# Optimization experiments

Measured on AMD Instinct MI355X. Metric: run time of the kernel, lower is better.

The kernel has to match this reference:

```python
import jax, jax.numpy as jnp
import numpy as np

D = 768; H = 12; DH = D // H; L = 12; FF = 3072; P = 20
IMG = (640, 360); NP_ = (IMG[0] // P) * (IMG[1] // P)  # 576 patches
NC = 10
EPS = 1e-5


def setup_inputs() -> dict:
    key = jax.random.key(0)
    ks = jax.random.split(key, 20)
    s = 0.02
    inp = {
        "x": jax.random.normal(ks[0], (16, 3, IMG[0], IMG[1]), jnp.float32),
        "patch_w": jax.random.normal(ks[1], (D, 3, P, P), jnp.float32) * s,
        "patch_b": jnp.zeros((D,), jnp.float32),
        "pos_emb": jax.random.normal(ks[2], (1, NP_, D), jnp.float32),
        "ln_g": jnp.ones((D,), jnp.float32),
        "ln_b": jnp.zeros((D,), jnp.float32),
        "Wq": jax.random.normal(ks[3], (L, D, D), jnp.float32) * s,
        "bq": jnp.zeros((L, D), jnp.float32),
        "Wk": jax.random.normal(ks[4], (L, D, D), jnp.float32) * s,
        "bk": jnp.zeros((L, D), jnp.float32),
        "Wv": jax.random.normal(ks[5], (L, D, D), jnp.float32) * s,
        "bv": jnp.zeros((L, D), jnp.float32),
        "Wo": jax.random.normal(ks[6], (L, D, D), jnp.float32) * s,
        "bo": jnp.zeros((L, D), jnp.float32),
        "W1": jax.random.normal(ks[7], (L, FF, D), jnp.float32) * s,
        "b1": jnp.zeros((L, FF), jnp.float32),
        "W2": jax.random.normal(ks[8], (L, D, FF), jnp.float32) * s,
        "b2": jnp.zeros((L, D), jnp.float32),
        "fc_w": jax.random.normal(ks[9], (NC, D), jnp.float32) * s,
        "fc_b": jnp.zeros((NC,), jnp.float32),
    }
    return inp


def _layer_norm(x, g, b):
    mu = jnp.mean(x, axis=-1, keepdims=True)
    var = jnp.mean(jnp.square(x - mu), axis=-1, keepdims=True)
    return (x - mu) * jax.lax.rsqrt(var + EPS) * g + b


def _forward(x, patch_w, patch_b, pos_emb, ln_g, ln_b,
             Wq, bq, Wk, bk, Wv, bv, Wo, bo, W1, b1, W2, b2, fc_w, fc_b):
    B = x.shape[0]
    Hp, Wp = IMG[0] // P, IMG[1] // P
    # patch embed: stride=kernel conv == per-patch linear
    patches = x.reshape(B, 3, Hp, P, Wp, P).transpose(0, 2, 4, 1, 3, 5)
    patches = patches.reshape(B, Hp * Wp, 3 * P * P)           # [B, N, 3*p*p]
    h = patches @ patch_w.reshape(D, -1).T + patch_b            # [B, N, D]
    h = h + pos_emb
    h = _layer_norm(h, ln_g, ln_b)

    def layer(h, p):
        wq, bq_, wk, bk_, wv, bv_, wo, bo_, w1, b1_, w2, b2_ = p
        N = h.shape[1]
        def heads(t):  # [B,N,D] -> [B,H,N,DH]
            return t.reshape(B, N, H, DH).transpose(0, 2, 1, 3)
        q = heads(h @ wq.T + bq_)
        k = heads(h @ wk.T + bk_)
        v = heads(h @ wv.T + bv_)
        scores = jnp.einsum('bhqd,bhkd->bhqk', q, k) / jnp.sqrt(jnp.float32(DH))
        attn = jax.nn.softmax(scores, axis=-1)
        o = jnp.einsum('bhqk,bhkd->bhqd', attn, v)
        o = o.transpose(0, 2, 1, 3).reshape(B, N, D) @ wo.T + bo_
        h = h + o
        ff = jax.nn.relu(h @ w1.T + b1_) @ w2.T + b2_
        return h + ff, None

    h, _ = jax.lax.scan(layer, h, (Wq, bq, Wk, bk, Wv, bv, Wo, bo, W1, b1, W2, b2))
    pooled = h.mean(axis=1)                                     # [B, D]
    return pooled @ fc_w.T + fc_b                               # [B, NC]


def reference(x, patch_w, patch_b, pos_emb, ln_g, ln_b,
              Wq, bq, Wk, bk, Wv, bv, Wo, bo, W1, b1, W2, b2, fc_w, fc_b):
    return _forward(x, patch_w, patch_b, pos_emb, ln_g, ln_b,
                    Wq, bq, Wk, bk, Wv, bv, Wo, bo, W1, b1, W2, b2, fc_w, fc_b)
```

## Files before the change

### kernel.cpp

```cpp
#include <hip/hip_runtime.h>
#include <stdint.h>
#include <stddef.h>

typedef __attribute__((ext_vector_type(8))) short short8;
typedef __attribute__((ext_vector_type(4))) float f32x4;

#define D_    768
#define HH    12
#define DHEAD 64
#define NP    576
#define BB    16
#define MROWS 9216
#define KPAT  1216
#define SCL   0.18033688011112042f

static __device__ __forceinline__ unsigned short f2bf(float f){
  union { float f; unsigned int u; } v; v.f = f;
  unsigned int u = v.u;
  return (unsigned short)((u + 0x7FFFu + ((u >> 16) & 1u)) >> 16);
}

static __device__ __forceinline__ void gld16(const void* g, void* l){
  __builtin_amdgcn_global_load_lds((const __attribute__((address_space(1))) void*)g,
                                   (__attribute__((address_space(3))) void*)l,
                                   16, 0, 0);
}

__global__ __launch_bounds__(256) void gemm_bt(
    const unsigned short* __restrict__ A,
    const unsigned short* __restrict__ W,
    const float* __restrict__ bias,
    const float* __restrict__ pos,
    const float* res,
    float* outf,
    unsigned short* outb,
    int M, int N, int K, int relu)
{
  __shared__ unsigned short sA[3][128*32];
  __shared__ unsigned short sB[3][128*32];
  const int NB = N >> 7;
  const int nwg = (int)gridDim.x;
  int wid = (int)blockIdx.x;
  wid = (wid & 7) * (nwg >> 3) + (wid >> 3);
  const int mb = wid / NB;
  const int nb = wid % NB;
  const int t = threadIdx.x;
  const int w = t >> 6, l = t & 63;
  const int m0 = mb << 7, n0 = nb << 7;

  const int srow = (w << 4) + (l >> 2);
  const int scb  = (l & 3) ^ ((l >> 3) & 3);
  const unsigned short* Ag = A + (size_t)(m0 + srow) * K + (scb << 3);
  const unsigned short* Wg = W + (size_t)(n0 + srow) * K + (scb << 3);
  const size_t g64 = (size_t)64 * K;

  const f32x4 zero = {0.f, 0.f, 0.f, 0.f};
  f32x4 acc[4][4];
  #pragma unroll
  for (int i = 0; i < 4; ++i)
    #pragma unroll
    for (int j = 0; j < 4; ++j) acc[i][j] = zero;

  const int KT = K >> 5;

  auto stage = [&](int kt){
    const int bf = kt % 3;
    const unsigned short* a0 = Ag + (size_t)kt * 32;
    const unsigned short* w0 = Wg + (size_t)kt * 32;
    gld16(a0,       &sA[bf][((w<<4) +  0)*32]);
    gld16(a0 + g64, &sA[bf][((w<<4) + 64)*32]);
    gld16(w0,       &sB[bf][((w<<4) +  0)*32]);
    gld16(w0 + g64, &sB[bf][((w<<4) + 64)*32]);
  };

  stage(0);
  stage(1);

  const int wr = w >> 1, wc = w & 1;
  const int fr = l & 15, fq = l >> 4;
  const int fsw = (fq ^ ((fr >> 1) & 3)) << 3;

  for (int kt = 0; kt < KT; ++kt){
    if (kt == KT - 1) asm volatile("s_waitcnt vmcnt(0) lgkmcnt(0)" ::: "memory");
    else              asm volatile("s_waitcnt vmcnt(4) lgkmcnt(0)" ::: "memory");
    __builtin_amdgcn_s_barrier();
    asm volatile("" ::: "memory");
    if (kt + 2 < KT) stage(kt + 2);
    const int buf = kt % 3;
    short8 af[4], bv[4];
    #pragma unroll
    for (int mf = 0; mf < 4; ++mf)
      af[mf] = *(const short8*)&sA[buf][((wr<<6) + (mf<<4) + fr)*32 + fsw];
    #pragma unroll
    for (int nf = 0; nf < 4; ++nf)
      bv[nf] = *(const short8*)&sB[buf][((wc<<6) + (nf<<4) + fr)*32 + fsw];
    #pragma unroll
    for (int mf = 0; mf < 4; ++mf)
      #pragma unroll
      for (int nf = 0; nf < 4; ++nf)
        acc[mf][nf] = __builtin_amdgcn_mfma_f32_16x16x32_bf16(af[mf], bv[nf], acc[mf][nf], 0, 0, 0);
    asm volatile("" ::: "memory");
  }

  #pragma unroll
  for (int mf = 0; mf < 4; ++mf){
    #pragma unroll
    for (int nf = 0; nf < 4; ++nf){
      #pragma unroll
      for (int r = 0; r < 4; ++r){
        const int row = m0 + (wr<<6) + (mf<<4) + (fq<<2) + r;
        const int col = n0 + (wc<<6) + (nf<<4) + fr;
        float v = acc[mf][nf][r] + bias[col];
        if (pos)  v += pos[(size_t)(row % NP) * D_ + col];
        if (res)  v += res[(size_t)row * N + col];
        if (relu) v = fmaxf(v, 0.f);
        const size_t idx = (size_t)row * N + col;
        if (outf) outf[idx] = v;
        if (outb) outb[idx] = f2bf(v);
      }
    }
  }
}

__global__ __launch_bounds__(384) void k_attn(const unsigned short* __restrict__ qkv,
                                              unsigned short* __restrict__ o)
{
  __shared__ unsigned short Kl[2][32*64];
  __shared__ unsigned short Vt[2][64*64];
  const int nwg = (int)gridDim.x;
  int wid = (int)blockIdx.x;
  wid = (wid & 7) * (nwg >> 3) + (wid >> 3);
  const int bh = wid / 3, qs = wid % 3;
  const int b = bh / HH, h = bh % HH;
  const unsigned short* base = qkv + (size_t)b * NP * 2304 + h * DHEAD;
  const int t = threadIdx.x;
  const int w = t >> 6, l = t & 63;
  const int fr = l & 15, fq = l >> 4;
  const int sg = l & 7;
  const int sr = ((w & 3) << 3) + (l >> 3);
  const bool stw = (t < 256);

  short8 qfa[2], qfb[2];
  #pragma unroll
  for (int qt = 0; qt < 2; ++qt){
    const size_t qrow = (size_t)(qs*192 + (qt*6 + w)*16 + fr);
    qfa[qt] = *(const short8*)(base + qrow*2304 + (fq<<3));
    qfb[qt] = *(const short8*)(base + qrow*2304 + 32 + (fq<<3));
  }

  const f32x4 zero = {0.f, 0.f, 0.f, 0.f};
  float mx_[2] = {-1e30f, -1e30f};
  float ls_[2] = {0.f, 0.f};
  f32x4 oa[2][4];
  #pragma unroll
  for (int qt = 0; qt < 2; ++qt)
    #pragma unroll
    for (int nf = 0; nf < 4; ++nf) oa[qt][nf] = zero;

  if (stw){
    gld16(base + 768 + (size_t)sr*2304 + ((sg ^ (sr&7))<<3), &Kl[0][(w&3)*512]);
    short8 vv = *(const short8*)(base + 1536 + (size_t)sr*2304 + (sg<<3));
    asm volatile("s_waitcnt vmcnt(0)" ::: "memory");
    #pragma unroll
    for (int j = 0; j < 8; ++j){
      const int d = sg*8 + j;
      const int off = (d<<7) + ((((sr>>3) ^ j ^ sg) & 7) << 4) + ((sr&7)<<1);
      *(unsigned short*)((char*)&Vt[0][0] + off) = ((const unsigned short*)&vv)[j];
    }
  }
  __syncthreads();

  for (int kt = 0; kt < 18; ++kt){
    const int buf = kt & 1;
    short8 vv;
    const bool st = stw && (kt < 17);
    if (st){
      const int key = (kt+1)*32 + sr;
      gld16(base + 768 + (size_t)key*2304 + ((sg ^ (sr&7))<<3), &Kl[buf^1][(w&3)*512]);
      vv = *(const short8*)(base + 1536 + (size_t)key*2304 + (sg<<3));
    }

    const char* kb = (const char*)&Kl[buf][0];
    const int r0 = fr, r1 = 16 + fr;
    const short8 k00 = *(const short8*)(kb + (r0<<7) + (((fq    ) ^ (r0&7))<<4));
    const short8 k01 = *(const short8*)(kb + (r0<<7) + (((4+fq ) ^ (r0&7))<<4));
    const short8 k10 = *(const short8*)(kb + (r1<<7) + (((fq    ) ^ (r1&7))<<4));
    const short8 k11 = *(const short8*)(kb + (r1<<7) + (((4+fq ) ^ (r1&7))<<4));
    const char* vb = (const char*)&Vt[buf][0];

    #pragma unroll
    for (int qt = 0; qt < 2; ++qt){
      f32x4 s0 = zero, s1 = zero;
      s0 = __builtin_amdgcn_mfma_f32_16x16x32_bf16(k00, qfa[qt], s0, 0, 0, 0);
      s0 = __builtin_amdgcn_mfma_f32_16x16x32_bf16(k01, qfb[qt], s0, 0, 0, 0);
      s1 = __builtin_amdgcn_mfma_f32_16x16x32_bf16(k10, qfa[qt], s1, 0, 0, 0);
      s1 = __builtin_amdgcn_mfma_f32_16x16x32_bf16(k11, qfb[qt], s1, 0, 0, 0);
      float mx = fmaxf(fmaxf(fmaxf(s0[0], s0[1]), fmaxf(s0[2], s0[3])),
                       fmaxf(fmaxf(s1[0], s1[1]), fmaxf(s1[2], s1[3])));
      mx = fmaxf(mx, __shfl_xor(mx, 16));
      mx = fmaxf(mx, __shfl_xor(mx, 32));
      const float mn = fmaxf(mx_[qt], mx * SCL);
      const float fc = exp2f(mx_[qt] - mn);
      const float p0 = exp2f(s0[0]*SCL - mn), p1 = exp2f(s0[1]*SCL - mn);
      const float p2 = exp2f(s0[2]*SCL - mn), p3 = exp2f(s0[3]*SCL - mn);
      const float p4 = exp2f(s1[0]*SCL - mn), p5 = exp2f(s1[1]*SCL - mn);
      const float p6 = exp2f(s1[2]*SCL - mn), p7 = exp2f(s1[3]*SCL - mn);
      float ps = ((p0+p1)+(p2+p3)) + ((p4+p5)+(p6+p7));
      ps += __shfl_xor(ps, 16);
      ps += __shfl_xor(ps, 32);
      ls_[qt] = ls_[qt] * fc + ps;
      mx_[qt] = mn;
      if (!__all(fc == 1.0f)){
        const float fA = __shfl(fc, (fq<<2) + 0);
        const float fB = __shfl(fc, (fq<<2) + 1);
        const float fC = __shfl(fc, (fq<<2) + 2);
        const float fD = __shfl(fc, (fq<<2) + 3);
        #pragma unroll
        for (int nf = 0; nf < 4; ++nf){
          oa[qt][nf][0] *= fA; oa[qt][nf][1] *= fB;
          oa[qt][nf][2] *= fC; oa[qt][nf][3] *= fD;
        }
      }
      unsigned d0, d1, d2, d3;
      asm("v_cvt_pk_bf16_f32 %0, %1, %2" : "=v"(d0) : "v"(p0), "v"(p1));
      asm("v_cvt_pk_bf16_f32 %0, %1, %2" : "=v"(d1) : "v"(p2), "v"(p3));
      asm("v_cvt_pk_bf16_f32 %0, %1, %2" : "=v"(d2) : "v"(p4), "v"(p5));
      asm("v_cvt_pk_bf16_f32 %0, %1, %2" : "=v"(d3) : "v"(p6), "v"(p7));
      const int srcA = fr + ((fq & 1) << 5);
      const unsigned a0 = (unsigned)__shfl((int)d0, srcA);
      const unsigned a1 = (unsigned)__shfl((int)d1, srcA);
      const unsigned a2 = (unsigned)__shfl((int)d2, srcA);
      const unsigned a3 = (unsigned)__shfl((int)d3, srcA);
      const unsigned b0 = (unsigned)__shfl((int)d0, srcA + 16);
      const unsigned b1 = (unsigned)__shfl((int)d1, srcA + 16);
      const unsigned b2 = (unsigned)__shfl((int)d2, srcA + 16);
      const unsigned b3 = (unsigned)__shfl((int)d3, srcA + 16);
      const bool hi = fq >= 2;
      union { unsigned u[4]; short8 v; } pk;
      pk.u[0] = hi ? a2 : a0;
      pk.u[1] = hi ? a3 : a1;
      pk.u[2] = hi ? b2 : b0;
      pk.u[3] = hi ? b3 : b1;
      const short8 pa = pk.v;
      #pragma unroll
      for (int nf = 0; nf < 4; ++nf){
        const int d = (nf<<4) + fr;
        const short8 vf = *(const short8*)(vb + (d<<7) + (((fq ^ (d&7) ^ (d>>3)) & 7)<<4));
        oa[qt][nf] = __builtin_amdgcn_mfma_f32_16x16x32_bf16(pa, vf, oa[qt][nf], 0, 0, 0);
      }
    }

    if (st){
      asm volatile("s_waitcnt vmcnt(0)" ::: "memory");
      #pragma unroll
      for (int j = 0; j < 8; ++j){
        const int d = sg*8 + j;
        const int off = (d<<7) + ((((sr>>3) ^ j ^ sg) & 7) << 4) + ((sr&7)<<1);
        *(unsigned short*)((char*)&Vt[buf^1][0] + off) = ((const unsigned short*)&vv)[j];
      }
    }
    __syncthreads();
  }

  #pragma unroll
  for (int qt = 0; qt < 2; ++qt){
    const float rl = 1.f / ls_[qt];
    const float rA = __shfl(rl, (fq<<2)+0), rB = __shfl(rl, (fq<<2)+1);
    const float rC = __shfl(rl, (fq<<2)+2), rD = __shfl(rl, (fq<<2)+3);
    const size_t r0 = (size_t)(b*NP + qs*192 + (qt*6 + w)*16 + (fq<<2));
    #pragma unroll
    for (int nf = 0; nf < 4; ++nf){
      const int col = h*DHEAD + (nf<<4) + fr;
      o[(r0 + 0)*D_ + col] = f2bf(oa[qt][nf][0] * rA);
      o[(r0 + 1)*D_ + col] = f2bf(oa[qt][nf][1] * rB);
      o[(r0 + 2)*D_ + col] = f2bf(oa[qt][nf][2] * rC);
      o[(r0 + 3)*D_ + col] = f2bf(oa[qt][nf][3] * rD);
    }
  }
}

__global__ void k_f2b(const float* __restrict__ s, unsigned short* __restrict__ d, long n){
  long i = (long)blockIdx.x * blockDim.x + threadIdx.x;
  const long st = (long)gridDim.x * blockDim.x;
  for (; i < n; i += st) d[i] = f2bf(s[i]);
}

__global__ void k_pack_qkvw(const float* __restrict__ Wq, const float* __restrict__ Wk,
                            const float* __restrict__ Wv, unsigned short* __restrict__ dst){
  const long n = (long)12 * 2304 * 768;
  long i = (long)blockIdx.x * blockDim.x + threadIdx.x;
  const long st = (long)gridDim.x * blockDim.x;
  for (; i < n; i += st){
    const int lay = (int)(i / (2304 * 768));
    const int rem = (int)(i % (2304 * 768));
    const int r = rem / 768, k = rem % 768;
    const float* s = (r < 768) ? Wq : ((r < 1536) ? Wk : Wv);
    const int rr = (r < 768) ? r : ((r < 1536) ? r - 768 : r - 1536);
    dst[i] = f2bf(s[(size_t)lay * 589824 + (size_t)rr * 768 + k]);
  }
}

__global__ void k_pack_qkvb(const float* __restrict__ bq, const float* __restrict__ bk,
                            const float* __restrict__ bv, float* __restrict__ dst){
  const int i = blockIdx.x * 256 + threadIdx.x;
  if (i >= 12 * 2304) return;
  const int lay = i / 2304, r = i % 2304;
  const float* s = (r < 768) ? bq : ((r < 1536) ? bk : bv);
  const int rr = (r < 768) ? r : ((r < 1536) ? r - 768 : r - 1536);
  dst[i] = s[lay * 768 + rr];
}

__global__ void k_patchw(const float* __restrict__ s, unsigned short* __restrict__ d){
  const long n = (long)768 * KPAT;
  long i = (long)blockIdx.x * blockDim.x + threadIdx.x;
  const long st = (long)gridDim.x * blockDim.x;
  for (; i < n; i += st){
    const int r = (int)(i / KPAT), k = (int)(i % KPAT);
    d[i] = (k < 1200) ? f2bf(s[(size_t)r * 1200 + k]) : (unsigned short)0;
  }
}

__global__ void k_patches(const float* __restrict__ x, unsigned short* __restrict__ d){
  const long n = (long)MROWS * KPAT;
  long i = (long)blockIdx.x * blockDim.x + threadIdx.x;
  const long st = (long)gridDim.x * blockDim.x;
  for (; i < n; i += st){
    const int mrow = (int)(i / KPAT), k = (int)(i % KPAT);
    unsigned short v = 0;
    if (k < 1200){
      const int c = k / 400, rem = k % 400, py = rem / 20, px = rem % 20;
      const int b = mrow / NP, pn = mrow % NP, hp = pn / 18, wp = pn % 18;
      v = f2bf(x[(((size_t)b * 3 + c) * 640 + hp * 20 + py) * 360 + wp * 20 + px]);
    }
    d[i] = v;
  }
}

__global__ __launch_bounds__(256) void k_ln(float* h, unsigned short* hb,
                                            const float* __restrict__ g,
                                            const float* __restrict__ bt){
  const int r = blockIdx.x, t = threadIdx.x;
  const size_t base = (size_t)r * D_;
  const float x0 = h[base + t], x1 = h[base + t + 256], x2 = h[base + t + 512];
  float s = x0 + x1 + x2;
  #pragma unroll
  for (int o = 1; o < 64; o <<= 1) s += __shfl_xor(s, o);
  __shared__ float red[8];
  const int w = t >> 6, l = t & 63;
  if (l == 0) red[w] = s;
  __syncthreads();
  const float mu = (red[0] + red[1] + red[2] + red[3]) * (1.f / 768.f);
  const float d0 = x0 - mu, d1 = x1 - mu, d2 = x2 - mu;
  float v = d0*d0 + d1*d1 + d2*d2;
  #pragma unroll
  for (int o = 1; o < 64; o <<= 1) v += __shfl_xor(v, o);
  if (l == 0) red[4 + w] = v;
  __syncthreads();
  const float var = (red[4] + red[5] + red[6] + red[7]) * (1.f / 768.f);
  const float rs = rsqrtf(var + 1e-5f);
  const float y0 = d0 * rs * g[t]       + bt[t];
  const float y1 = d1 * rs * g[t + 256] + bt[t + 256];
  const float y2 = d2 * rs * g[t + 512] + bt[t + 512];
  h[base + t] = y0; h[base + t + 256] = y1; h[base + t + 512] = y2;
  hb[base + t] = f2bf(y0); hb[base + t + 256] = f2bf(y1); hb[base + t + 512] = f2bf(y2);
}

__global__ void k_pool(const float* __restrict__ h, float* __restrict__ p){
  const int i = blockIdx.x * 256 + threadIdx.x;
  const int b = i / D_, c = i % D_;
  const float* base = h + (size_t)b * NP * D_ + c;
  float s = 0.f;
  for (int n = 0; n < NP; ++n) s += base[(size_t)n * D_];
  p[i] = s * (1.f / 576.f);
}

__global__ __launch_bounds__(64) void k_fc(const float* __restrict__ p, const float* __restrict__ w,
                                           const float* __restrict__ bias, float* __restrict__ out){
  const int oi = blockIdx.x;
  const int b = oi / 10, j = oi % 10;
  const int l = threadIdx.x;
  float s = 0.f;
  for (int c = l; c < D_; c += 64) s += p[b * D_ + c] * w[j * D_ + c];
  #pragma unroll
  for (int o = 1; o < 64; o <<= 1) s += __shfl_xor(s, o);
  if (l == 0) out[oi] = s + bias[j];
}

extern "C" void kernel_launch(void* const* d_in, const int* in_sizes, int n_in,
                              void* d_out, int out_size, void* d_ws, size_t ws_size,
                              hipStream_t stream)
{
  const float* x       = (const float*)d_in[0];
  const float* patch_w = (const float*)d_in[1];
  const float* patch_b = (const float*)d_in[2];
  const float* pos_emb = (const float*)d_in[3];
  const float* ln_g    = (const float*)d_in[4];
  const float* ln_b    = (const float*)d_in[5];
  const float* Wq      = (const float*)d_in[6];
  const float* bq      = (const float*)d_in[7];
  const float* Wk      = (const float*)d_in[8];
  const float* bk      = (const float*)d_in[9];
  const float* Wv      = (const float*)d_in[10];
  const float* bv      = (const float*)d_in[11];
  const float* Wo      = (const float*)d_in[12];
  const float* bo      = (const float*)d_in[13];
  const float* W1      = (const float*)d_in[14];
  const float* b1      = (const float*)d_in[15];
  const float* W2      = (const float*)d_in[16];
  const float* b2      = (const float*)d_in[17];
  const float* fc_w    = (const float*)d_in[18];
  const float* fc_b    = (const float*)d_in[19];
  float* out = (float*)d_out;
  (void)in_sizes; (void)n_in; (void)out_size; (void)ws_size;

  char* ws = (char*)d_ws;
  size_t off = 0;
  auto alloc = [&](size_t bytes) -> char* {
    char* p = ws + off;
    off += (bytes + 255) & ~(size_t)255;
    return p;
  };
  unsigned short* wqkv    = (unsigned short*)alloc((size_t)12*2304*768*2);
  unsigned short* wo      = (unsigned short*)alloc((size_t)12*768*768*2);
  unsigned short* w1      = (unsigned short*)alloc((size_t)12*3072*768*2);
  unsigned short* w2      = (unsigned short*)alloc((size_t)12*768*3072*2);
  unsigned short* wp      = (unsigned short*)alloc((size_t)768*KPAT*2);
  float*          bqkv    = (float*)alloc((size_t)12*2304*4);
  unsigned short* patches = (unsigned short*)alloc((size_t)MROWS*KPAT*2);
  float*          hf      = (float*)alloc((size_t)MROWS*D_*4);
  unsigned short* hb      = (unsigned short*)alloc((size_t)MROWS*D_*2);
  unsigned short* qkvb    = (unsigned short*)alloc((size_t)MROWS*2304*2);
  unsigned short* ob      = (unsigned short*)alloc((size_t)MROWS*D_*2);
  unsigned short* ffb     = (unsigned short*)alloc((size_t)MROWS*3072*2);
  float*          pooled  = (float*)alloc((size_t)16*D_*4);

  k_pack_qkvw<<<2048, 256, 0, stream>>>(Wq, Wk, Wv, wqkv);
  k_pack_qkvb<<<(12*2304 + 255)/256, 256, 0, stream>>>(bq, bk, bv, bqkv);
  k_f2b<<<2048, 256, 0, stream>>>(Wo, wo, (long)12*768*768);
  k_f2b<<<2048, 256, 0, stream>>>(W1, w1, (long)12*3072*768);
  k_f2b<<<2048, 256, 0, stream>>>(W2, w2, (long)12*768*3072);
  k_patchw<<<2048, 256, 0, stream>>>(patch_w, wp);
  k_patches<<<2048, 256, 0, stream>>>(x, patches);

  gemm_bt<<<72*6, 256, 0, stream>>>(patches, wp, patch_b, pos_emb,
                                    nullptr, hf, nullptr, MROWS, 768, KPAT, 0);
  k_ln<<<MROWS, 256, 0, stream>>>(hf, hb, ln_g, ln_b);

  for (int l = 0; l < 12; ++l){
    gemm_bt<<<72*18, 256, 0, stream>>>(hb, wqkv + (size_t)l*2304*768, bqkv + l*2304,
                                       nullptr, nullptr, nullptr, qkvb, MROWS, 2304, 768, 0);
    k_attn<<<576, 384, 0, stream>>>(qkvb, ob);
    gemm_bt<<<72*6, 256, 0, stream>>>(ob, wo + (size_t)l*768*768, bo + l*768,
                                      nullptr, hf, hf, hb, MROWS, 768, 768, 0);
    gemm_bt<<<72*24, 256, 0, stream>>>(hb, w1 + (size_t)l*3072*768, b1 + (size_t)l*3072,
                                       nullptr, nullptr, nullptr, ffb, MROWS, 3072, 768, 1);
    gemm_bt<<<72*6, 256, 0, stream>>>(ffb, w2 + (size_t)l*768*3072, b2 + l*768,
                                      nullptr, hf, hf, hb, MROWS, 768, 3072, 0);
  }
  k_pool<<<48, 256, 0, stream>>>(hf, pooled);
  k_fc<<<160, 64, 0, stream>>>(pooled, fc_w, fc_b, out);
}
```

Before: 4.258 ms.

## Enlarge GEMM tile to 256x128 with K-step 64 and 8 waves

Reworks the bf16 GEMM to use 512-thread workgroups, each computing a 256x128 output tile with a 64-wide K step. The shared-memory layout changes to 64-column rows with an XOR swizzle. Global-to-LDS loads are reorganised to six per stage, and MFMA bursts are wrapped in s_setprio. The goal is more operand reuse per byte loaded and fewer barrier iterations. In exchange, about 147KB of LDS is needed, so only one block fits per CU, and grids get smaller.

```diff
diff --git a/kernel.cpp b/kernel.cpp
--- a/kernel.cpp
+++ b/kernel.cpp
@@ -26,7 +26,7 @@
                                    16, 0, 0);
 }
 
-__global__ __launch_bounds__(256) void gemm_bt(
+__global__ __launch_bounds__(512) void gemm_bt(
     const unsigned short* __restrict__ A,
     const unsigned short* __restrict__ W,
     const float* __restrict__ bias,
@@ -36,8 +36,8 @@
     unsigned short* outb,
     int M, int N, int K, int relu)
 {
-  __shared__ unsigned short sA[3][128*32];
-  __shared__ unsigned short sB[3][128*32];
+  __shared__ unsigned short sA[3][256*64];
+  __shared__ unsigned short sB[3][128*64];
   const int NB = N >> 7;
   const int nwg = (int)gridDim.x;
   int wid = (int)blockIdx.x;
@@ -46,13 +46,18 @@
   const int nb = wid % NB;
   const int t = threadIdx.x;
   const int w = t >> 6, l = t & 63;
-  const int m0 = mb << 7, n0 = nb << 7;
-
-  const int srow = (w << 4) + (l >> 2);
-  const int scb  = (l & 3) ^ ((l >> 3) & 3);
-  const unsigned short* Ag = A + (size_t)(m0 + srow) * K + (scb << 3);
-  const unsigned short* Wg = W + (size_t)(n0 + srow) * K + (scb << 3);
-  const size_t g64 = (size_t)64 * K;
+  const int m0 = mb << 8, n0 = nb << 7;
+
+  const int lr = l >> 3;
+  const int sch = (l & 7) ^ lr;
+  const unsigned short* aP[4];
+  const unsigned short* bP[2];
+  #pragma unroll
+  for (int i = 0; i < 4; ++i)
+    aP[i] = A + (size_t)(m0 + (((i<<3)+w)<<3) + lr) * K + (sch<<3);
+  #pragma unroll
+  for (int i = 0; i < 2; ++i)
+    bP[i] = W + (size_t)(n0 + (((i<<3)+w)<<3) + lr) * K + (sch<<3);
 
   const f32x4 zero = {0.f, 0.f, 0.f, 0.f};
   f32x4 acc[4][4];
@@ -61,16 +66,17 @@
     #pragma unroll
     for (int j = 0; j < 4; ++j) acc[i][j] = zero;
 
-  const int KT = K >> 5;
+  const int KT = K >> 6;
 
   auto stage = [&](int kt){
     const int bf = kt % 3;
-    const unsigned short* a0 = Ag + (size_t)kt * 32;
-    const unsigned short* w0 = Wg + (size_t)kt * 32;
-    gld16(a0,       &sA[bf][((w<<4) +  0)*32]);
-    gld16(a0 + g64, &sA[bf][((w<<4) + 64)*32]);
-    gld16(w0,       &sB[bf][((w<<4) +  0)*32]);
-    gld16(w0 + g64, &sB[bf][((w<<4) + 64)*32]);
+    const size_t ko = (size_t)kt << 6;
+    #pragma unroll
+    for (int i = 0; i < 4; ++i)
+      gld16(aP[i] + ko, &sA[bf][(((i<<3)+w)<<9)]);
+    #pragma unroll
+    for (int i = 0; i < 2; ++i)
+      gld16(bP[i] + ko, &sB[bf][(((i<<3)+w)<<9)]);
   };
 
   stage(0);
@@ -78,27 +84,36 @@
 
   const int wr = w >> 1, wc = w & 1;
   const int fr = l & 15, fq = l >> 4;
-  const int fsw = (fq ^ ((fr >> 1) & 3)) << 3;
 
   for (int kt = 0; kt < KT; ++kt){
-    if (kt == KT - 1) asm volatile("s_waitcnt vmcnt(0) lgkmcnt(0)" ::: "memory");
-    else              asm volatile("s_waitcnt vmcnt(4) lgkmcnt(0)" ::: "memory");
+    if (kt == KT - 1) asm volatile("s_waitcnt vmcnt(0)" ::: "memory");
+    else              asm volatile("s_waitcnt vmcnt(6)" ::: "memory");
     __builtin_amdgcn_s_barrier();
     asm volatile("" ::: "memory");
     if (kt + 2 < KT) stage(kt + 2);
     const int buf = kt % 3;
-    short8 af[4], bv[4];
-    #pragma unroll
-    for (int mf = 0; mf < 4; ++mf)
-      af[mf] = *(const short8*)&sA[buf][((wr<<6) + (mf<<4) + fr)*32 + fsw];
-    #pragma unroll
-    for (int nf = 0; nf < 4; ++nf)
-      bv[nf] = *(const short8*)&sB[buf][((wc<<6) + (nf<<4) + fr)*32 + fsw];
-    #pragma unroll
-    for (int mf = 0; mf < 4; ++mf)
-      #pragma unroll
-      for (int nf = 0; nf < 4; ++nf)
-        acc[mf][nf] = __builtin_amdgcn_mfma_f32_16x16x32_bf16(af[mf], bv[nf], acc[mf][nf], 0, 0, 0);
+    #pragma unroll
+    for (int kc = 0; kc < 2; ++kc){
+      const int ch = (kc << 2) + fq;
+      short8 af[4], bv[4];
+      #pragma unroll
+      for (int mf = 0; mf < 4; ++mf){
+        const int r = (wr<<6) + (mf<<4) + fr;
+        af[mf] = *(const short8*)&sA[buf][(r<<6) + ((ch ^ (r&7))<<3)];
+      }
+      #pragma unroll
+      for (int nf = 0; nf < 4; ++nf){
+        const int c = (wc<<6) + (nf<<4) + fr;
+        bv[nf] = *(const short8*)&sB[buf][(c<<6) + ((ch ^ (c&7))<<3)];
+      }
+      __builtin_amdgcn_s_setprio(1);
+      #pragma unroll
+      for (int mf = 0; mf < 4; ++mf)
+        #pragma unroll
+        for (int nf = 0; nf < 4; ++nf)
+          acc[mf][nf] = __builtin_amdgcn_mfma_f32_16x16x32_bf16(af[mf], bv[nf], acc[mf][nf], 0, 0, 0);
+      __builtin_amdgcn_s_setprio(0);
+    }
     asm volatile("" ::: "memory");
   }
 
@@ -442,19 +457,19 @@
   k_patchw<<<2048, 256, 0, stream>>>(patch_w, wp);
   k_patches<<<2048, 256, 0, stream>>>(x, patches);
 
-  gemm_bt<<<72*6, 256, 0, stream>>>(patches, wp, patch_b, pos_emb,
+  gemm_bt<<<36*6, 512, 0, stream>>>(patches, wp, patch_b, pos_emb,
                                     nullptr, hf, nullptr, MROWS, 768, KPAT, 0);
   k_ln<<<MROWS, 256, 0, stream>>>(hf, hb, ln_g, ln_b);
 
   for (int l = 0; l < 12; ++l){
-    gemm_bt<<<72*18, 256, 0, stream>>>(hb, wqkv + (size_t)l*2304*768, bqkv + l*2304,
+    gemm_bt<<<36*18, 512, 0, stream>>>(hb, wqkv + (size_t)l*2304*768, bqkv + l*2304,
                                        nullptr, nullptr, nullptr, qkvb, MROWS, 2304, 768, 0);
     k_attn<<<576, 384, 0, stream>>>(qkvb, ob);
-    gemm_bt<<<72*6, 256, 0, stream>>>(ob, wo + (size_t)l*768*768, bo + l*768,
+    gemm_bt<<<36*6, 512, 0, stream>>>(ob, wo + (size_t)l*768*768, bo + l*768,
                                       nullptr, hf, hf, hb, MROWS, 768, 768, 0);
-    gemm_bt<<<72*24, 256, 0, stream>>>(hb, w1 + (size_t)l*3072*768, b1 + (size_t)l*3072,
+    gemm_bt<<<36*24, 512, 0, stream>>>(hb, w1 + (size_t)l*3072*768, b1 + (size_t)l*3072,
                                        nullptr, nullptr, nullptr, ffb, MROWS, 3072, 768, 1);
-    gemm_bt<<<72*6, 256, 0, stream>>>(ffb, w2 + (size_t)l*768*3072, b2 + l*768,
+    gemm_bt<<<36*6, 512, 0, stream>>>(ffb, w2 + (size_t)l*768*3072, b2 + l*768,
                                       nullptr, hf, hf, hb, MROWS, 768, 3072, 0);
   }
   k_pool<<<48, 256, 0, stream>>>(hf, pooled);
```

New measurement: 4.582 ms. +7.6%, slower.

## Restructure GEMM to keep weight slab in LDS and stream A from global

Applied to the files above, without the earlier changes.

Rewrites the bf16 GEMM so each 512-thread block loads a 64-column by up-to-768-K slab of the weight matrix into a 128KB LDS buffer once, with an XOR swizzle. A fragments are then read directly from global memory into registers, software-pipelined four k-steps deep. Tiles become 256x64 instead of 128x128, and KPAT is padded to 1280 so the patch GEMM splits into 768-wide chunks. The aim is to remove the per-k-step LDS staging and barriers for A, at the cost of uncoalesced global A reads, very high LDS use that limits occupancy, and a changed padded patch layout.

```diff
diff --git a/kernel.cpp b/kernel.cpp
--- a/kernel.cpp
+++ b/kernel.cpp
@@ -11,7 +11,7 @@
 #define NP    576
 #define BB    16
 #define MROWS 9216
-#define KPAT  1216
+#define KPAT  1280
 #define SCL   0.18033688011112042f
 
 static __device__ __forceinline__ unsigned short f2bf(float f){
@@ -26,7 +26,7 @@
                                    16, 0, 0);
 }
 
-__global__ __launch_bounds__(256) void gemm_bt(
+__global__ __launch_bounds__(512) void gemm_bt(
     const unsigned short* __restrict__ A,
     const unsigned short* __restrict__ W,
     const float* __restrict__ bias,
@@ -36,9 +36,8 @@
     unsigned short* outb,
     int M, int N, int K, int relu)
 {
-  __shared__ unsigned short sA[3][128*32];
-  __shared__ unsigned short sB[3][128*32];
-  const int NB = N >> 7;
+  __shared__ unsigned short sW[64*1024];
+  const int NB = N >> 6;
   const int nwg = (int)gridDim.x;
   int wid = (int)blockIdx.x;
   wid = (wid & 7) * (nwg >> 3) + (wid >> 3);
@@ -46,70 +45,80 @@
   const int nb = wid % NB;
   const int t = threadIdx.x;
   const int w = t >> 6, l = t & 63;
-  const int m0 = mb << 7, n0 = nb << 7;
-
-  const int srow = (w << 4) + (l >> 2);
-  const int scb  = (l & 3) ^ ((l >> 3) & 3);
-  const unsigned short* Ag = A + (size_t)(m0 + srow) * K + (scb << 3);
-  const unsigned short* Wg = W + (size_t)(n0 + srow) * K + (scb << 3);
-  const size_t g64 = (size_t)64 * K;
-
-  const f32x4 zero = {0.f, 0.f, 0.f, 0.f};
-  f32x4 acc[4][4];
-  #pragma unroll
-  for (int i = 0; i < 4; ++i)
-    #pragma unroll
-    for (int j = 0; j < 4; ++j) acc[i][j] = zero;
-
-  const int KT = K >> 5;
-
-  auto stage = [&](int kt){
-    const int bf = kt % 3;
-    const unsigned short* a0 = Ag + (size_t)kt * 32;
-    const unsigned short* w0 = Wg + (size_t)kt * 32;
-    gld16(a0,       &sA[bf][((w<<4) +  0)*32]);
-    gld16(a0 + g64, &sA[bf][((w<<4) + 64)*32]);
-    gld16(w0,       &sB[bf][((w<<4) +  0)*32]);
-    gld16(w0 + g64, &sB[bf][((w<<4) + 64)*32]);
-  };
-
-  stage(0);
-  stage(1);
-
+  const int m0 = mb << 8, n0 = nb << 6;
   const int wr = w >> 1, wc = w & 1;
   const int fr = l & 15, fq = l >> 4;
-  const int fsw = (fq ^ ((fr >> 1) & 3)) << 3;
-
-  for (int kt = 0; kt < KT; ++kt){
-    if (kt == KT - 1) asm volatile("s_waitcnt vmcnt(0) lgkmcnt(0)" ::: "memory");
-    else              asm volatile("s_waitcnt vmcnt(4) lgkmcnt(0)" ::: "memory");
-    __builtin_amdgcn_s_barrier();
-    asm volatile("" ::: "memory");
-    if (kt + 2 < KT) stage(kt + 2);
-    const int buf = kt % 3;
-    short8 af[4], bv[4];
-    #pragma unroll
-    for (int mf = 0; mf < 4; ++mf)
-      af[mf] = *(const short8*)&sA[buf][((wr<<6) + (mf<<4) + fr)*32 + fsw];
-    #pragma unroll
-    for (int nf = 0; nf < 4; ++nf)
-      bv[nf] = *(const short8*)&sB[buf][((wc<<6) + (nf<<4) + fr)*32 + fsw];
-    #pragma unroll
-    for (int mf = 0; mf < 4; ++mf)
-      #pragma unroll
-      for (int nf = 0; nf < 4; ++nf)
-        acc[mf][nf] = __builtin_amdgcn_mfma_f32_16x16x32_bf16(af[mf], bv[nf], acc[mf][nf], 0, 0, 0);
-    asm volatile("" ::: "memory");
+
+  const unsigned short* rowA[4];
+  #pragma unroll
+  for (int mf = 0; mf < 4; ++mf)
+    rowA[mf] = A + (size_t)(m0 + (wr<<6) + (mf<<4) + fr) * K;
+
+  const f32x4 zero = {0.f, 0.f, 0.f, 0.f};
+  f32x4 acc[4][2];
+  #pragma unroll
+  for (int i = 0; i < 4; ++i){ acc[i][0] = zero; acc[i][1] = zero; }
+
+  for (int k0 = 0; k0 < K; k0 += 768){
+    const int KS = (K - k0 < 768) ? (K - k0) : 768;
+    const int NS = KS >> 5;
+    const int HPR = (KS > 512) ? 2 : 1;
+
+    if (k0) __syncthreads();
+    for (int i = w; i < (HPR << 6); i += 8){
+      const int c = (HPR == 2) ? (i >> 1) : i;
+      const int h = (HPR == 2) ? (i & 1) : 0;
+      int ci = (h << 6) + l;
+      ci ^= (c & 7);
+      int eo = ci << 3;
+      if (eo >= KS) eo = 0;
+      gld16(W + (size_t)(n0 + c) * K + k0 + eo, &sW[c*1024 + (h<<9)]);
+    }
+    __syncthreads();
+
+    auto LA = [&](short8* a, int ks){
+      const int ko = k0 + (ks << 5) + (fq << 3);
+      #pragma unroll
+      for (int mf = 0; mf < 4; ++mf) a[mf] = *(const short8*)(rowA[mf] + ko);
+    };
+    auto LB = [&](short8* b, int ks){
+      const int ch = (ks << 2) + fq;
+      #pragma unroll
+      for (int nf = 0; nf < 2; ++nf){
+        const int c = (wc << 5) + (nf << 4) + fr;
+        b[nf] = *(const short8*)&sW[c*1024 + ((ch ^ (c & 7)) << 3)];
+      }
+    };
+    auto MM = [&](short8* a, short8* b){
+      #pragma unroll
+      for (int mf = 0; mf < 4; ++mf)
+        #pragma unroll
+        for (int nf = 0; nf < 2; ++nf)
+          acc[mf][nf] = __builtin_amdgcn_mfma_f32_16x16x32_bf16(a[mf], b[nf], acc[mf][nf], 0, 0, 0);
+    };
+
+    short8 a0[4], a1[4], a2[4], a3[4];
+    short8 b0[2], b1[2], b2[2], b3[2];
+    LA(a0, 0); LB(b0, 0);
+    LA(a1, 1); LB(b1, 1);
+    LA(a2, 2); LB(b2, 2);
+    LA(a3, 3); LB(b3, 3);
+    for (int ks = 0; ks < NS; ks += 4){
+      MM(a0, b0); if (ks + 4 < NS){ LA(a0, ks + 4); LB(b0, ks + 4); }
+      MM(a1, b1); if (ks + 5 < NS){ LA(a1, ks + 5); LB(b1, ks + 5); }
+      MM(a2, b2); if (ks + 6 < NS){ LA(a2, ks + 6); LB(b2, ks + 6); }
+      MM(a3, b3); if (ks + 7 < NS){ LA(a3, ks + 7); LB(b3, ks + 7); }
+    }
   }
 
   #pragma unroll
   for (int mf = 0; mf < 4; ++mf){
     #pragma unroll
-    for (int nf = 0; nf < 4; ++nf){
+    for (int nf = 0; nf < 2; ++nf){
       #pragma unroll
       for (int r = 0; r < 4; ++r){
         const int row = m0 + (wr<<6) + (mf<<4) + (fq<<2) + r;
-        const int col = n0 + (wc<<6) + (nf<<4) + fr;
+        const int col = n0 + (wc<<5) + (nf<<4) + fr;
         float v = acc[mf][nf][r] + bias[col];
         if (pos)  v += pos[(size_t)(row % NP) * D_ + col];
         if (res)  v += res[(size_t)row * N + col];
@@ -442,20 +451,20 @@
   k_patchw<<<2048, 256, 0, stream>>>(patch_w, wp);
   k_patches<<<2048, 256, 0, stream>>>(x, patches);
 
-  gemm_bt<<<72*6, 256, 0, stream>>>(patches, wp, patch_b, pos_emb,
-                                    nullptr, hf, nullptr, MROWS, 768, KPAT, 0);
+  gemm_bt<<<36*12, 512, 0, stream>>>(patches, wp, patch_b, pos_emb,
+                                     nullptr, hf, nullptr, MROWS, 768, KPAT, 0);
   k_ln<<<MROWS, 256, 0, stream>>>(hf, hb, ln_g, ln_b);
 
   for (int l = 0; l < 12; ++l){
-    gemm_bt<<<72*18, 256, 0, stream>>>(hb, wqkv + (size_t)l*2304*768, bqkv + l*2304,
+    gemm_bt<<<36*36, 512, 0, stream>>>(hb, wqkv + (size_t)l*2304*768, bqkv + l*2304,
                                        nullptr, nullptr, nullptr, qkvb, MROWS, 2304, 768, 0);
     k_attn<<<576, 384, 0, stream>>>(qkvb, ob);
-    gemm_bt<<<72*6, 256, 0, stream>>>(ob, wo + (size_t)l*768*768, bo + l*768,
-                                      nullptr, hf, hf, hb, MROWS, 768, 768, 0);
-    gemm_bt<<<72*24, 256, 0, stream>>>(hb, w1 + (size_t)l*3072*768, b1 + (size_t)l*3072,
+    gemm_bt<<<36*12, 512, 0, stream>>>(ob, wo + (size_t)l*768*768, bo + l*768,
+                                       nullptr, hf, hf, hb, MROWS, 768, 768, 0);
+    gemm_bt<<<36*48, 512, 0, stream>>>(hb, w1 + (size_t)l*3072*768, b1 + (size_t)l*3072,
                                        nullptr, nullptr, nullptr, ffb, MROWS, 3072, 768, 1);
-    gemm_bt<<<72*6, 256, 0, stream>>>(ffb, w2 + (size_t)l*768*3072, b2 + l*768,
-                                      nullptr, hf, hf, hb, MROWS, 768, 3072, 0);
+    gemm_bt<<<36*12, 512, 0, stream>>>(ffb, w2 + (size_t)l*768*3072, b2 + l*768,
+                                       nullptr, hf, hf, hb, MROWS, 768, 3072, 0);
   }
   k_pool<<<48, 256, 0, stream>>>(hf, pooled);
   k_fc<<<160, 64, 0, stream>>>(pooled, fc_w, fc_b, out);
```

Measured after the change: 9.555 ms. 124% more time.
